# Kernel tuning notes

Hardware: AMD Instinct MI355X
Metric: run time of the kernel (lower is better)

Reference implementation:

```python
import jax, jax.numpy as jnp
import numpy as np
from jax import lax

T, B, I, N, C, L = 512, 256, 64, 512, 10, 3
TAU = 2.0  # train_tau=False -> constant, non-trainable


def setup_inputs() -> dict:
    key = jax.random.key(0)
    ks = jax.random.split(key, 12)
    f32 = jnp.float32
    data = jax.random.normal(ks[0], (T, B, I), f32)
    h0 = 0.1 * jax.random.uniform(ks[1], (L, B, N), f32)  # matches 0.1*torch.rand init
    # Linear params; weights stored as [in, out] so y = x @ W + b
    Win = jax.random.normal(ks[2], (I, N), f32) / np.float32(np.sqrt(I))
    b_in = 0.01 * jax.random.normal(ks[3], (N,), f32)
    Whh = jax.random.normal(ks[4], (L, N, N), f32) / np.float32(np.sqrt(N))
    b_hh = 0.01 * jax.random.normal(ks[5], (L, N), f32)
    Whi = jax.random.normal(ks[6], (L - 1, N, N), f32) / np.float32(np.sqrt(N))
    b_hi = 0.01 * jax.random.normal(ks[7], (L - 1, N), f32)
    Wfc = jax.random.normal(ks[8], (N, C), f32) / np.float32(np.sqrt(N))
    b_fc = 0.01 * jax.random.normal(ks[9], (C,), f32)
    return {"data": data, "h0": h0, "Win": Win, "b_in": b_in,
            "Whh": Whh, "b_hh": b_hh, "Whi": Whi, "b_hi": b_hi,
            "Wfc": Wfc, "b_fc": b_fc}


def reference(data, h0, Win, b_in, Whh, b_hh, Whi, b_hi, Wfc, b_fc):
    alpha = 1.0 - 1.0 / TAU
    # forward() zeroes the recurrent diagonal every call
    Whh = Whh * (1.0 - jnp.eye(N, dtype=Whh.dtype))
    x = data @ Win + b_in  # [T, B, N] input projection (single input layer, mean over 1)

    def step(hs, inp):
        h0_, h1_, h2_ = hs
        # layer 0: leaky integration + LeakyReLU; same inp fed to every layer
        n0 = jax.nn.leaky_relu(alpha * h0_ + (h0_ @ Whh[0] + b_hh[0] + inp) / TAU)
        # layer 1 sees the *updated* layer-0 state (sequential within a timestep)
        n1 = jax.nn.leaky_relu(
            alpha * h1_ + (h1_ @ Whh[1] + b_hh[1] + n0 @ Whi[0] + b_hi[0] + inp) / TAU)
        n2 = jax.nn.leaky_relu(
            alpha * h2_ + (h2_ @ Whh[2] + b_hh[2] + n1 @ Whi[1] + b_hi[1] + inp) / TAU)
        return (n0, n1, n2), None

    hs_final, _ = lax.scan(step, (h0[0], h0[1], h0[2]), x)
    out = hs_final[-1] @ Wfc + b_fc  # [B, C], single readout head
    return out
```

## Files before the change

### kernel.cpp

```cpp
#include <hip/hip_runtime.h>
#include <stdint.h>


#define TS    512
#define BB    256
#define NN    512
#define MR    16
#define NRG   16
#define NCT   4
#define RD    8
#define LROW  520

typedef __attribute__((ext_vector_type(8))) short s8v;
typedef __attribute__((ext_vector_type(4))) float f4v;
typedef __attribute__((ext_vector_type(4))) unsigned int u4v;

#define MFMA16(a, b, c) __builtin_amdgcn_mfma_f32_16x16x32_bf16((a), (b), (c), 0, 0, 0)

__device__ __forceinline__ short f2bf(float f) {
  union { float f; unsigned u; } v; v.f = f;
  unsigned u = v.u;
  u += 0x7fffu + ((u >> 16) & 1u);
  return (short)(u >> 16);
}

__device__ __forceinline__ s8v pack8(f4v a, f4v b) {
  s8v v;
  v[0] = f2bf(a[0]); v[1] = f2bf(a[1]); v[2] = f2bf(a[2]); v[3] = f2bf(a[3]);
  v[4] = f2bf(b[0]); v[5] = f2bf(b[1]); v[6] = f2bf(b[2]); v[7] = f2bf(b[3]);
  return v;
}

__device__ __forceinline__ void ld8_sync(u4v o[8], const unsigned short* qp,
                                         const unsigned short* pp) {
  asm volatile(
      "global_load_dwordx4 %0, %8, off sc1\n\t"
      "global_load_dwordx4 %1, %8, off offset:16 sc1\n\t"
      "global_load_dwordx4 %2, %8, off offset:32 sc1\n\t"
      "global_load_dwordx4 %3, %8, off offset:48 sc1\n\t"
      "global_load_dwordx4 %4, %9, off sc1\n\t"
      "global_load_dwordx4 %5, %9, off offset:16 sc1\n\t"
      "global_load_dwordx4 %6, %9, off offset:32 sc1\n\t"
      "global_load_dwordx4 %7, %9, off offset:48 sc1\n\t"
      "s_waitcnt vmcnt(0)"
      : "=&v"(o[0]), "=&v"(o[1]), "=&v"(o[2]), "=&v"(o[3]),
        "=&v"(o[4]), "=&v"(o[5]), "=&v"(o[6]), "=&v"(o[7])
      : "v"(qp), "v"(pp)
      : "memory");
}
__device__ __forceinline__ void ld4_sync(u4v o[4], const unsigned short* p) {
  asm volatile(
      "global_load_dwordx4 %0, %4, off sc1\n\t"
      "global_load_dwordx4 %1, %4, off offset:16 sc1\n\t"
      "global_load_dwordx4 %2, %4, off offset:32 sc1\n\t"
      "global_load_dwordx4 %3, %4, off offset:48 sc1\n\t"
      "s_waitcnt vmcnt(0)"
      : "=&v"(o[0]), "=&v"(o[1]), "=&v"(o[2]), "=&v"(o[3])
      : "v"(p)
      : "memory");
}

__device__ __forceinline__ void stg_sc1_b16(unsigned short* p, unsigned v) {
  asm volatile("global_store_short %0, %1, off sc1" :: "v"(p), "v"(v) : "memory");
}
__device__ __forceinline__ void waitvm0() {
  asm volatile("s_waitcnt vmcnt(0)" ::: "memory");
}

__global__ __launch_bounds__(256, 1) void rnn_pipe(
    const float* __restrict__ data, const float* __restrict__ h0,
    const float* __restrict__ Win,  const float* __restrict__ b_in,
    const float* __restrict__ Whh,  const float* __restrict__ b_hh,
    const float* __restrict__ Whi,  const float* __restrict__ b_hi,
    unsigned short* __restrict__ ring, unsigned* __restrict__ cnt,
    float* __restrict__ hfinal)
{
  __shared__ __attribute__((aligned(16))) unsigned short qtile[MR * LROW];
  __shared__ __attribute__((aligned(16))) unsigned short ptile[MR * LROW];

  const int bi   = blockIdx.x;
  const int lay  = bi % 3;
  const int rest = bi / 3;
  const int rg   = rest & 15;
  const int ct   = rest >> 4;
  const int tid  = threadIdx.x;
  const int wv   = tid >> 6;
  const int lane = tid & 63;
  const int lo   = lane & 15;
  const int q4   = lane >> 4;
  const int row0 = rg * MR;
  const int cw   = ct * 128 + wv * 32;

  const int sidx = (lay * NRG + rg) * NCT + ct;
  unsigned* selfprod = cnt + (size_t)sidx * 32;
  unsigned* selfdone = cnt + (size_t)(256 + sidx) * 32;

  unsigned* pollptr = selfprod;
  int polltype = 0;
  if (lane < 4) {
    pollptr = cnt + (size_t)((lay * NRG + rg) * NCT + lane) * 32;  polltype = 1;
  } else if (lane >= 4 && lane < 8 && lay > 0) {
    pollptr = cnt + (size_t)(((lay - 1) * NRG + rg) * NCT + (lane - 4)) * 32;  polltype = 2;
  } else if (lane >= 8 && lane < 12 && lay < 2) {
    pollptr = cnt + (size_t)(256 + ((lay + 1) * NRG + rg) * NCT + (lane - 8)) * 32;  polltype = 3;
  }

  s8v WH[16][2];
  s8v WI[16][2];
  s8v WX[2][2];
  float biasv[2];
  f4v  hst[2];

  {
    const float* WmH = Whh + (size_t)lay * NN * NN;
    #pragma unroll
    for (int kk = 0; kk < 16; ++kk) {
      #pragma unroll
      for (int nf = 0; nf < 2; ++nf) {
        const int col = cw + nf * 16 + lo;
        s8v v;
        #pragma unroll
        for (int j = 0; j < 8; ++j) {
          const int k = kk * 32 + q4 * 8 + j;
          float f = WmH[(size_t)k * NN + col];
          if (k == col) f = 0.f;
          v[j] = f2bf(f);
        }
        WH[kk][nf] = v;
      }
    }
    if (lay > 0) {
      const float* WmI = Whi + (size_t)(lay - 1) * NN * NN;
      #pragma unroll
      for (int kk = 0; kk < 16; ++kk) {
        #pragma unroll
        for (int nf = 0; nf < 2; ++nf) {
          const int col = cw + nf * 16 + lo;
          s8v v;
          #pragma unroll
          for (int j = 0; j < 8; ++j)
            v[j] = f2bf(WmI[(size_t)(kk * 32 + q4 * 8 + j) * NN + col]);
          WI[kk][nf] = v;
        }
      }
    }
    #pragma unroll
    for (int kk = 0; kk < 2; ++kk) {
      #pragma unroll
      for (int nf = 0; nf < 2; ++nf) {
        const int col = cw + nf * 16 + lo;
        s8v v;
        #pragma unroll
        for (int j = 0; j < 8; ++j)
          v[j] = f2bf(Win[(size_t)(kk * 32 + q4 * 8 + j) * NN + col]);
        WX[kk][nf] = v;
      }
    }
    #pragma unroll
    for (int nf = 0; nf < 2; ++nf) {
      const int col = cw + nf * 16 + lo;
      float b = b_hh[lay * NN + col] + b_in[col];
      if (lay > 0) b += b_hi[(lay - 1) * NN + col];
      biasv[nf] = b;
      #pragma unroll
      for (int r = 0; r < 4; ++r)
        hst[nf][r] = h0[(size_t)lay * BB * NN + (size_t)(row0 + q4 * 4 + r) * NN + col];
    }
  }

  const size_t myring = (size_t)(lay * NRG + rg) * RD;
  const size_t upring = (size_t)((lay - 1) * NRG + rg) * RD;

  f4v xa0, xa1, xa2, xa3;
  {
    const float* dsrc = data + ((size_t)0 * BB + row0 + lo) * 64 + q4 * 8;
    xa0 = *(const f4v*)(dsrc + 0);
    xa1 = *(const f4v*)(dsrc + 4);
    xa2 = *(const f4v*)(dsrc + 32);
    xa3 = *(const f4v*)(dsrc + 36);
  }

  for (int t = 0; t < TS; ++t) {
    f4v zero4 = {0.f, 0.f, 0.f, 0.f};
    f4v acc[2] = {zero4, zero4};
    {
      s8v xv0 = pack8(xa0, xa1);
      s8v xv1 = pack8(xa2, xa3);
      acc[0] = MFMA16(xv0, WX[0][0], acc[0]);
      acc[1] = MFMA16(xv0, WX[0][1], acc[1]);
      acc[0] = MFMA16(xv1, WX[1][0], acc[0]);
      acc[1] = MFMA16(xv1, WX[1][1], acc[1]);
    }

    unsigned tgt = 0;
    if (polltype == 1) tgt = (unsigned)t;
    else if (polltype == 2) tgt = (unsigned)(t + 1);
    else if (polltype == 3 && t >= RD) tgt = (unsigned)(t - RD + 1);
    for (;;) {
      unsigned v = __hip_atomic_load(pollptr, __ATOMIC_RELAXED, __HIP_MEMORY_SCOPE_AGENT);
      if (__all((int)(v >= tgt))) break;
    }

    {
      const unsigned short* qsrc =
          ring + (myring + ((t - 1) & (RD - 1))) * (MR * NN) + (size_t)tid * 32;
      const unsigned short* psrc =
          ring + (upring + (t & (RD - 1))) * (MR * NN) + (size_t)tid * 32;
      u4v st[8];
      if (t >= 1 && lay > 0) {
        ld8_sync(st, qsrc, psrc);
        #pragma unroll
        for (int i = 0; i < 4; ++i) {
          const int c = tid * 4 + i;
          *(u4v*)(qtile + (c >> 6) * LROW + (c & 63) * 8) = st[i];
          *(u4v*)(ptile + (c >> 6) * LROW + (c & 63) * 8) = st[4 + i];
        }
      } else if (t >= 1) {
        ld4_sync(st, qsrc);
        #pragma unroll
        for (int i = 0; i < 4; ++i) {
          const int c = tid * 4 + i;
          *(u4v*)(qtile + (c >> 6) * LROW + (c & 63) * 8) = st[i];
        }
      } else if (lay > 0) {
        ld4_sync(st, psrc);
        #pragma unroll
        for (int i = 0; i < 4; ++i) {
          const int c = tid * 4 + i;
          *(u4v*)(ptile + (c >> 6) * LROW + (c & 63) * 8) = st[i];
        }
      }
    }
    __syncthreads();
    if (tid == 0 && lay > 0)
      __hip_atomic_store(selfdone, (unsigned)(t + 1), __ATOMIC_RELAXED,
                         __HIP_MEMORY_SCOPE_AGENT);

    if (lay > 0) {
      #pragma unroll
      for (int kk = 0; kk < 16; ++kk) {
        s8v av = *(const s8v*)(ptile + lo * LROW + kk * 32 + q4 * 8);
        acc[0] = MFMA16(av, WI[kk][0], acc[0]);
        acc[1] = MFMA16(av, WI[kk][1], acc[1]);
      }
    }
    if (t == 0) {
      const float* hsrc = h0 + (size_t)lay * BB * NN + (size_t)(row0 + lo) * NN + q4 * 8;
      #pragma unroll
      for (int kk = 0; kk < 16; ++kk) {
        f4v a = *(const f4v*)(hsrc + kk * 32);
        f4v b = *(const f4v*)(hsrc + kk * 32 + 4);
        s8v av = pack8(a, b);
        acc[0] = MFMA16(av, WH[kk][0], acc[0]);
        acc[1] = MFMA16(av, WH[kk][1], acc[1]);
      }
    } else {
      #pragma unroll
      for (int kk = 0; kk < 16; ++kk) {
        s8v av = *(const s8v*)(qtile + lo * LROW + kk * 32 + q4 * 8);
        acc[0] = MFMA16(av, WH[kk][0], acc[0]);
        acc[1] = MFMA16(av, WH[kk][1], acc[1]);
      }
    }

    {
      unsigned short* rslot = ring + (myring + (t & (RD - 1))) * (MR * NN);
      #pragma unroll
      for (int nf = 0; nf < 2; ++nf) {
        const int col = cw + nf * 16 + lo;
        #pragma unroll
        for (int r = 0; r < 4; ++r) {
          const int row = q4 * 4 + r;
          float v = 0.5f * hst[nf][r] + 0.5f * (acc[nf][r] + biasv[nf]);
          v = (v >= 0.f) ? v : 0.01f * v;
          hst[nf][r] = v;
          stg_sc1_b16(rslot + (size_t)row * NN + col,
                      (unsigned)(unsigned short)f2bf(v));
          if (lay == 2 && t == TS - 1)
            hfinal[(size_t)(row0 + row) * NN + col] = v;
        }
      }
    }

    {
      const int tn = (t + 1 < TS) ? t + 1 : t;
      const float* dsrc = data + ((size_t)tn * BB + row0 + lo) * 64 + q4 * 8;
      xa0 = *(const f4v*)(dsrc + 0);
      xa1 = *(const f4v*)(dsrc + 4);
      xa2 = *(const f4v*)(dsrc + 32);
      xa3 = *(const f4v*)(dsrc + 36);
    }
    waitvm0();
    __syncthreads();
    if (tid == 0)
      __hip_atomic_store(selfprod, (unsigned)(t + 1), __ATOMIC_RELAXED,
                         __HIP_MEMORY_SCOPE_AGENT);
  }
}

__global__ void readout_k(const float* __restrict__ hfinal, const float* __restrict__ Wfc,
                          const float* __restrict__ b_fc, float* __restrict__ out)
{
  const int row = blockIdx.x;
  const int lane = threadIdx.x;
  float a[10];
  #pragma unroll
  for (int c = 0; c < 10; ++c) a[c] = 0.f;
  for (int k = lane; k < NN; k += 64) {
    const float h = hfinal[(size_t)row * NN + k];
    const float* w = Wfc + (size_t)k * 10;
    #pragma unroll
    for (int c = 0; c < 10; ++c) a[c] += h * w[c];
  }
  #pragma unroll
  for (int off = 32; off > 0; off >>= 1) {
    #pragma unroll
    for (int c = 0; c < 10; ++c) a[c] += __shfl_down(a[c], off);
  }
  if (lane == 0) {
    #pragma unroll
    for (int c = 0; c < 10; ++c) out[row * 10 + c] = a[c] + b_fc[c];
  }
}

extern "C" void kernel_launch(void* const* d_in, const int* in_sizes, int n_in,
                              void* d_out, int out_size, void* d_ws, size_t ws_size,
                              hipStream_t stream) {
  (void)in_sizes; (void)n_in; (void)out_size; (void)ws_size;
  const float* data = (const float*)d_in[0];
  const float* h0   = (const float*)d_in[1];
  const float* Win  = (const float*)d_in[2];
  const float* b_in = (const float*)d_in[3];
  const float* Whh  = (const float*)d_in[4];
  const float* b_hh = (const float*)d_in[5];
  const float* Whi  = (const float*)d_in[6];
  const float* b_hi = (const float*)d_in[7];
  const float* Wfc  = (const float*)d_in[8];
  const float* b_fc = (const float*)d_in[9];

  unsigned short* ring = (unsigned short*)d_ws;
  const size_t ring_bytes = (size_t)3 * NRG * RD * MR * NN * 2;
  unsigned* cnt = (unsigned*)((char*)d_ws + ring_bytes);
  float* hfinal = (float*)((char*)d_ws + ring_bytes + 65536);

  hipMemsetAsync(cnt, 0, 65536, stream);
  hipLaunchKernelGGL(rnn_pipe, dim3(192), dim3(256), 0, stream,
                     data, h0, Win, b_in, Whh, b_hh, Whi, b_hi, ring, cnt, hfinal);
  hipLaunchKernelGGL(readout_k, dim3(256), dim3(64), 0, stream,
                     hfinal, Wfc, b_fc, (float*)d_out);
}
```

Measured before the change: 2.339 ms.

## Swizzle LDS tiles, coalesce ring loads, split MFMA accumulator chains

Replaces the padded LDS row layout with an XOR-swizzled layout to avoid bank conflicts without padding. Ring loads now use per-thread coalesced 16-byte offsets from a scalar base, so consecutive threads read consecutive chunks instead of each thread reading 64 contiguous bytes. The input and recurrent MFMAs now accumulate into one register set and the inter-layer MFMAs into a second set, summed at the end. This breaks the serial MFMA dependency chain so the two chains can interleave, at the cost of extra accumulator registers.

```diff
diff --git a/kernel.cpp b/kernel.cpp
--- a/kernel.cpp
+++ b/kernel.cpp
@@ -9,7 +9,8 @@
 #define NRG   16
 #define NCT   4
 #define RD    8
-#define LROW  520
+
+#define SW(r, c) (((r) << 9) + ((((c) ^ ((r) & 7))) << 3))
 
 typedef __attribute__((ext_vector_type(8))) short s8v;
 typedef __attribute__((ext_vector_type(4))) float f4v;
@@ -31,32 +32,35 @@
   return v;
 }
 
-__device__ __forceinline__ void ld8_sync(u4v o[8], const unsigned short* qp,
-                                         const unsigned short* pp) {
+__device__ __forceinline__ void ld8_sync(u4v o[8],
+    unsigned v0, unsigned v1, unsigned v2, unsigned v3,
+    const unsigned short* sq, const unsigned short* sp) {
   asm volatile(
-      "global_load_dwordx4 %0, %8, off sc1\n\t"
-      "global_load_dwordx4 %1, %8, off offset:16 sc1\n\t"
-      "global_load_dwordx4 %2, %8, off offset:32 sc1\n\t"
-      "global_load_dwordx4 %3, %8, off offset:48 sc1\n\t"
-      "global_load_dwordx4 %4, %9, off sc1\n\t"
-      "global_load_dwordx4 %5, %9, off offset:16 sc1\n\t"
-      "global_load_dwordx4 %6, %9, off offset:32 sc1\n\t"
-      "global_load_dwordx4 %7, %9, off offset:48 sc1\n\t"
+      "global_load_dwordx4 %0, %8, %12 sc1\n\t"
+      "global_load_dwordx4 %1, %9, %12 sc1\n\t"
+      "global_load_dwordx4 %2, %10, %12 sc1\n\t"
+      "global_load_dwordx4 %3, %11, %12 sc1\n\t"
+      "global_load_dwordx4 %4, %8, %13 sc1\n\t"
+      "global_load_dwordx4 %5, %9, %13 sc1\n\t"
+      "global_load_dwordx4 %6, %10, %13 sc1\n\t"
+      "global_load_dwordx4 %7, %11, %13 sc1\n\t"
       "s_waitcnt vmcnt(0)"
       : "=&v"(o[0]), "=&v"(o[1]), "=&v"(o[2]), "=&v"(o[3]),
         "=&v"(o[4]), "=&v"(o[5]), "=&v"(o[6]), "=&v"(o[7])
-      : "v"(qp), "v"(pp)
+      : "v"(v0), "v"(v1), "v"(v2), "v"(v3), "s"(sq), "s"(sp)
       : "memory");
 }
-__device__ __forceinline__ void ld4_sync(u4v o[4], const unsigned short* p) {
+__device__ __forceinline__ void ld4_sync(u4v o[4],
+    unsigned v0, unsigned v1, unsigned v2, unsigned v3,
+    const unsigned short* sb) {
   asm volatile(
-      "global_load_dwordx4 %0, %4, off sc1\n\t"
-      "global_load_dwordx4 %1, %4, off offset:16 sc1\n\t"
-      "global_load_dwordx4 %2, %4, off offset:32 sc1\n\t"
-      "global_load_dwordx4 %3, %4, off offset:48 sc1\n\t"
+      "global_load_dwordx4 %0, %4, %8 sc1\n\t"
+      "global_load_dwordx4 %1, %5, %8 sc1\n\t"
+      "global_load_dwordx4 %2, %6, %8 sc1\n\t"
+      "global_load_dwordx4 %3, %7, %8 sc1\n\t"
       "s_waitcnt vmcnt(0)"
       : "=&v"(o[0]), "=&v"(o[1]), "=&v"(o[2]), "=&v"(o[3])
-      : "v"(p)
+      : "v"(v0), "v"(v1), "v"(v2), "v"(v3), "s"(sb)
       : "memory");
 }
 
@@ -75,8 +79,8 @@
     unsigned short* __restrict__ ring, unsigned* __restrict__ cnt,
     float* __restrict__ hfinal)
 {
-  __shared__ __attribute__((aligned(16))) unsigned short qtile[MR * LROW];
-  __shared__ __attribute__((aligned(16))) unsigned short ptile[MR * LROW];
+  __shared__ __attribute__((aligned(16))) unsigned short qtile[MR * NN];
+  __shared__ __attribute__((aligned(16))) unsigned short ptile[MR * NN];
 
   const int bi   = blockIdx.x;
   const int lay  = bi % 3;
@@ -171,6 +175,11 @@
   const size_t myring = (size_t)(lay * NRG + rg) * RD;
   const size_t upring = (size_t)((lay - 1) * NRG + rg) * RD;
 
+  unsigned voff0 = (unsigned)((0 * 256 + tid) * 16);
+  unsigned voff1 = (unsigned)((1 * 256 + tid) * 16);
+  unsigned voff2 = (unsigned)((2 * 256 + tid) * 16);
+  unsigned voff3 = (unsigned)((3 * 256 + tid) * 16);
+
   f4v xa0, xa1, xa2, xa3;
   {
     const float* dsrc = data + ((size_t)0 * BB + row0 + lo) * 64 + q4 * 8;
@@ -182,14 +191,15 @@
 
   for (int t = 0; t < TS; ++t) {
     f4v zero4 = {0.f, 0.f, 0.f, 0.f};
-    f4v acc[2] = {zero4, zero4};
+    f4v accQ[2] = {zero4, zero4};
+    f4v accP[2] = {zero4, zero4};
     {
       s8v xv0 = pack8(xa0, xa1);
       s8v xv1 = pack8(xa2, xa3);
-      acc[0] = MFMA16(xv0, WX[0][0], acc[0]);
-      acc[1] = MFMA16(xv0, WX[0][1], acc[1]);
-      acc[0] = MFMA16(xv1, WX[1][0], acc[0]);
-      acc[1] = MFMA16(xv1, WX[1][1], acc[1]);
+      accQ[0] = MFMA16(xv0, WX[0][0], accQ[0]);
+      accQ[1] = MFMA16(xv0, WX[0][1], accQ[1]);
+      accQ[0] = MFMA16(xv1, WX[1][0], accQ[0]);
+      accQ[1] = MFMA16(xv1, WX[1][1], accQ[1]);
     }
 
     unsigned tgt = 0;
@@ -202,32 +212,33 @@
     }
 
     {
-      const unsigned short* qsrc =
-          ring + (myring + ((t - 1) & (RD - 1))) * (MR * NN) + (size_t)tid * 32;
-      const unsigned short* psrc =
-          ring + (upring + (t & (RD - 1))) * (MR * NN) + (size_t)tid * 32;
+      const unsigned short* qsrc = ring + (myring + ((t - 1) & (RD - 1))) * (MR * NN);
+      const unsigned short* psrc = ring + (upring + (t & (RD - 1))) * (MR * NN);
       u4v st[8];
       if (t >= 1 && lay > 0) {
-        ld8_sync(st, qsrc, psrc);
+        ld8_sync(st, voff0, voff1, voff2, voff3, qsrc, psrc);
         #pragma unroll
         for (int i = 0; i < 4; ++i) {
-          const int c = tid * 4 + i;
-          *(u4v*)(qtile + (c >> 6) * LROW + (c & 63) * 8) = st[i];
-          *(u4v*)(ptile + (c >> 6) * LROW + (c & 63) * 8) = st[4 + i];
+          const int g = i * 256 + tid;
+          const int r = g >> 6, c = g & 63;
+          *(u4v*)(qtile + SW(r, c)) = st[i];
+          *(u4v*)(ptile + SW(r, c)) = st[4 + i];
         }
       } else if (t >= 1) {
-        ld4_sync(st, qsrc);
+        ld4_sync(st, voff0, voff1, voff2, voff3, qsrc);
         #pragma unroll
         for (int i = 0; i < 4; ++i) {
-          const int c = tid * 4 + i;
-          *(u4v*)(qtile + (c >> 6) * LROW + (c & 63) * 8) = st[i];
+          const int g = i * 256 + tid;
+          const int r = g >> 6, c = g & 63;
+          *(u4v*)(qtile + SW(r, c)) = st[i];
         }
       } else if (lay > 0) {
-        ld4_sync(st, psrc);
+        ld4_sync(st, voff0, voff1, voff2, voff3, psrc);
         #pragma unroll
         for (int i = 0; i < 4; ++i) {
-          const int c = tid * 4 + i;
-          *(u4v*)(ptile + (c >> 6) * LROW + (c & 63) * 8) = st[i];
+          const int g = i * 256 + tid;
+          const int r = g >> 6, c = g & 63;
+          *(u4v*)(ptile + SW(r, c)) = st[i];
         }
       }
     }
@@ -239,9 +250,9 @@
     if (lay > 0) {
       #pragma unroll
       for (int kk = 0; kk < 16; ++kk) {
-        s8v av = *(const s8v*)(ptile + lo * LROW + kk * 32 + q4 * 8);
-        acc[0] = MFMA16(av, WI[kk][0], acc[0]);
-        acc[1] = MFMA16(av, WI[kk][1], acc[1]);
+        s8v av = *(const s8v*)(ptile + SW(lo, kk * 4 + q4));
+        accP[0] = MFMA16(av, WI[kk][0], accP[0]);
+        accP[1] = MFMA16(av, WI[kk][1], accP[1]);
       }
     }
     if (t == 0) {
@@ -251,15 +262,15 @@
         f4v a = *(const f4v*)(hsrc + kk * 32);
         f4v b = *(const f4v*)(hsrc + kk * 32 + 4);
         s8v av = pack8(a, b);
-        acc[0] = MFMA16(av, WH[kk][0], acc[0]);
-        acc[1] = MFMA16(av, WH[kk][1], acc[1]);
+        accQ[0] = MFMA16(av, WH[kk][0], accQ[0]);
+        accQ[1] = MFMA16(av, WH[kk][1], accQ[1]);
       }
     } else {
       #pragma unroll
       for (int kk = 0; kk < 16; ++kk) {
-        s8v av = *(const s8v*)(qtile + lo * LROW + kk * 32 + q4 * 8);
-        acc[0] = MFMA16(av, WH[kk][0], acc[0]);
-        acc[1] = MFMA16(av, WH[kk][1], acc[1]);
+        s8v av = *(const s8v*)(qtile + SW(lo, kk * 4 + q4));
+        accQ[0] = MFMA16(av, WH[kk][0], accQ[0]);
+        accQ[1] = MFMA16(av, WH[kk][1], accQ[1]);
       }
     }
 
@@ -271,7 +282,7 @@
         #pragma unroll
         for (int r = 0; r < 4; ++r) {
           const int row = q4 * 4 + r;
-          float v = 0.5f * hst[nf][r] + 0.5f * (acc[nf][r] + biasv[nf]);
+          float v = 0.5f * hst[nf][r] + 0.5f * (accQ[nf][r] + accP[nf][r] + biasv[nf]);
           v = (v >= 0.f) ? v : 0.01f * v;
           hst[nf][r] = v;
           stg_sc1_b16(rslot + (size_t)row * NN + col,
```

Result: faster. 2.240 ms (-4.2%).
